# Kernel optimization log

Measured on AMD Instinct MI355X. Metric: run time of the kernel, lower is better.

Reference implementation:

```python
import math
import jax, jax.numpy as jnp
import numpy as np

N_EXPERTS = 8
TOP_K = 2
CAP_FACTOR = 1.25

def _capacity(num_tokens: int) -> int:
    cap = math.floor(TOP_K * CAP_FACTOR * num_tokens / N_EXPERTS)
    cap += cap % 2
    return max(int(cap), 2)

def setup_inputs() -> dict:
    key = jax.random.key(0)
    k1, k2 = jax.random.split(key)
    x = jax.random.normal(k1, (2, 2048, 1024), dtype=jnp.float32)
    w_gate = jax.random.normal(k2, (N_EXPERTS, 1024), dtype=jnp.float32) * 0.02
    return {"x": x, "w_gate": w_gate}

def reference(x, w_gate):
    B, S, D = x.shape
    N = B * S
    E, K = N_EXPERTS, TOP_K
    cap = _capacity(N)

    xf = x.astype(jnp.float32)
    router_logits = jnp.einsum('bsd,ed->bse', xf, w_gate)  # [B,S,E]
    lf = router_logits.reshape(N, E)

    # top-k gating: softmax over only the top-k logits (others -inf)
    topv, topi = jax.lax.top_k(lf, K)                       # [N,K]
    masked = jnp.full((N, E), -jnp.inf, dtype=lf.dtype)
    masked = masked.at[jnp.arange(N)[:, None], topi].set(topv)
    router_probs = jax.nn.softmax(masked, axis=-1)          # [N,E]

    # per-(k,token) expert one-hot, ranked by global cumsum order (k-major)
    mask = jax.nn.one_hot(topi, E, dtype=jnp.int32)         # [N,K,E]
    mask = jnp.transpose(mask, (1, 0, 2))                   # [K,N,E]
    rank = jnp.cumsum(mask.reshape(K * N, E), axis=0) - 1   # position within each expert
    rank = rank.reshape(K, N, E)
    mask = mask * (rank < cap)                              # drop tokens over capacity
    rank_k = jnp.sum(mask * rank, axis=-1)                  # [K,N] slot index per assignment

    weights = mask.astype(router_probs.dtype) * router_probs[None]   # [K,N,E]
    rank_oh = jax.nn.one_hot(rank_k, cap, dtype=router_probs.dtype)  # [K,N,cap]
    # sum over k of outer(weights[k,n,:], rank_oh[k,n,:]) -> [N,E,cap]
    expert_weights = jnp.einsum('kne,knc->nec', weights, rank_oh)
    expert_mask = expert_weights > 0                        # [N,E,cap] bool

    x_flat = x.reshape(N, D)
    # gather token features into expert batches: [E,cap,N] @ [N,D]
    expert_batches = jnp.einsum('nec,nd->ecd', expert_mask.astype(x.dtype), x_flat)

    return expert_weights, expert_mask, expert_batches, router_logits
```

## Files before the change

kernel.cpp:

```cpp
#include <hip/hip_runtime.h>
#include <hip/hip_bf16.h>
#include <math.h>

#define DIM 1024
#define NEXP 8

__global__ __launch_bounds__(256) void k_router(
    const float* __restrict__ x, const float* __restrict__ wg,
    float* __restrict__ logits,
    int* __restrict__ e1, int* __restrict__ e2,
    float* __restrict__ p1, float* __restrict__ p2, int N)
{
    __shared__ float wlds[NEXP * DIM];
    const int tid = threadIdx.x;
    for (int i = tid; i < NEXP * DIM; i += 256) wlds[i] = wg[i];
    __syncthreads();

    const int wave = tid >> 6, lane = tid & 63;
    const int n = blockIdx.x * 4 + wave;
    if (n >= N) return;

    const float4* x4 = (const float4*)x + (size_t)n * (DIM / 4);
    float s[NEXP];
#pragma unroll
    for (int e = 0; e < NEXP; ++e) s[e] = 0.0f;

#pragma unroll
    for (int i = 0; i < 4; ++i) {
        const int idx = lane + 64 * i;
        const float4 v = x4[idx];
#pragma unroll
        for (int e = 0; e < NEXP; ++e) {
            const float* wrow = &wlds[e * DIM + idx * 4];
            float acc = s[e];
            acc = fmaf(v.x, wrow[0], acc);
            acc = fmaf(v.y, wrow[1], acc);
            acc = fmaf(v.z, wrow[2], acc);
            acc = fmaf(v.w, wrow[3], acc);
            s[e] = acc;
        }
    }

#pragma unroll
    for (int off = 32; off >= 1; off >>= 1) {
#pragma unroll
        for (int e = 0; e < NEXP; ++e) s[e] += __shfl_xor(s[e], off, 64);
    }

    int be1 = 0; float bv1 = s[0];
#pragma unroll
    for (int e = 1; e < NEXP; ++e) { if (s[e] > bv1) { bv1 = s[e]; be1 = e; } }
    int be2 = -1; float bv2 = -INFINITY;
#pragma unroll
    for (int e = 0; e < NEXP; ++e) { if (e != be1 && s[e] > bv2) { bv2 = s[e]; be2 = e; } }

    const float t = expf(bv2 - bv1);
    const float inv = 1.0f / (1.0f + t);

    if (lane == 0) {
#pragma unroll
        for (int e = 0; e < NEXP; ++e) logits[(size_t)n * NEXP + e] = s[e];
        e1[n] = be1; e2[n] = be2;
        p1[n] = inv; p2[n] = t * inv;
    }
}

__global__ __launch_bounds__(1024) void k_scan(
    const int* __restrict__ e1, const int* __restrict__ e2,
    const float* __restrict__ p1, const float* __restrict__ p2,
    int* __restrict__ r_table, float* __restrict__ p_table,
    int* __restrict__ slot_token, int N, int cap)
{
    const int tid = threadIdx.x;
    for (int i = tid; i < N * NEXP; i += 1024) r_table[i] = -1;
    for (int i = tid; i < NEXP * cap; i += 1024) slot_token[i] = -1;
    __syncthreads();
    if (tid >= 64) return;

    const int lane = tid;
    const unsigned long long below =
        (lane == 0) ? 0ULL : ((~0ULL) >> (64 - lane));

    int cnt[NEXP];
#pragma unroll
    for (int q = 0; q < NEXP; ++q) cnt[q] = 0;

    const int rounds = N / 64;
    for (int k = 0; k < 2; ++k) {
        const int*   ee = (k == 0) ? e1 : e2;
        const float* pp = (k == 0) ? p1 : p2;
        for (int r = 0; r < rounds; ++r) {
            const int n = r * 64 + lane;
            const int e = ee[n];
            const float p = pp[n];
            int rank = 0x7fffffff;
#pragma unroll
            for (int q = 0; q < NEXP; ++q) {
                const unsigned long long bal = __ballot(e == q);
                if (e == q) rank = cnt[q] + __popcll(bal & below);
                cnt[q] += __popcll(bal);
            }
            if (rank < cap) {
                r_table[n * NEXP + e] = rank;
                p_table[n * NEXP + e] = p;
                slot_token[e * cap + rank] = n;
            }
        }
    }
}

__global__ __launch_bounds__(256) void k_fill_wm(
    const int* __restrict__ r_table, const float* __restrict__ p_table,
    float* __restrict__ W, float* __restrict__ M, int cap, int nrows)
{
    const int wave = threadIdx.x >> 6, lane = threadIdx.x & 63;
    const int row = blockIdx.x * 4 + wave;
    if (row >= nrows) return;

    const int r = r_table[row];
    const float p = p_table[row];
    const bool on = (r >= 0) && (p > 0.0f);

    if ((cap & 3) == 0) {
        float4* Wr = (float4*)(W + (size_t)row * cap);
        float4* Mr = (float4*)(M + (size_t)row * cap);
        const int nf4 = cap >> 2;
        for (int c4 = lane; c4 < nf4; c4 += 64) {
            const int c = c4 * 4;
            float4 w = make_float4(0.f, 0.f, 0.f, 0.f);
            float4 m = make_float4(0.f, 0.f, 0.f, 0.f);
            if (on) {
                const int d = r - c;
                if (d == 0)      { w.x = p; m.x = 1.f; }
                else if (d == 1) { w.y = p; m.y = 1.f; }
                else if (d == 2) { w.z = p; m.z = 1.f; }
                else if (d == 3) { w.w = p; m.w = 1.f; }
            }
            Wr[c4] = w; Mr[c4] = m;
        }
    } else {
        float* Wr = W + (size_t)row * cap;
        float* Mr = M + (size_t)row * cap;
        for (int c = lane; c < cap; c += 64) {
            const bool hit = on && (c == r);
            Wr[c] = hit ? p : 0.f;
            Mr[c] = hit ? 1.f : 0.f;
        }
    }
}

__global__ __launch_bounds__(256) void k_fill_batches(
    const int* __restrict__ slot_token, const float* __restrict__ x,
    float* __restrict__ Bt, int nrows)
{
    const int wave = threadIdx.x >> 6, lane = threadIdx.x & 63;
    const int row = blockIdx.x * 4 + wave;
    if (row >= nrows) return;

    const int tok = slot_token[row];
    float4* out = (float4*)(Bt + (size_t)row * DIM);
    if (tok >= 0) {
        const float4* src = (const float4*)(x + (size_t)tok * DIM);
#pragma unroll
        for (int i = 0; i < 4; ++i) out[lane + 64 * i] = src[lane + 64 * i];
    } else {
        const float4 z = make_float4(0.f, 0.f, 0.f, 0.f);
#pragma unroll
        for (int i = 0; i < 4; ++i) out[lane + 64 * i] = z;
    }
}

extern "C" void kernel_launch(void* const* d_in, const int* in_sizes, int n_in,
                              void* d_out, int out_size, void* d_ws, size_t ws_size,
                              hipStream_t stream)
{
    const float* x  = (const float*)d_in[0];
    const float* wg = (const float*)d_in[1];

    const int N = in_sizes[0] / DIM;
    int cap = (5 * N) / 16;
    cap += cap & 1;
    if (cap < 2) cap = 2;

    const size_t szW = (size_t)N * NEXP * cap;
    float* W  = (float*)d_out;
    float* M  = W + szW;
    float* Bt = M + szW;
    float* L  = Bt + (size_t)NEXP * cap * DIM;

    char* w = (char*)d_ws;
    int*   e1 = (int*)w;        w += (size_t)N * sizeof(int);
    int*   e2 = (int*)w;        w += (size_t)N * sizeof(int);
    float* p1 = (float*)w;      w += (size_t)N * sizeof(float);
    float* p2 = (float*)w;      w += (size_t)N * sizeof(float);
    int*   r_table = (int*)w;   w += (size_t)N * NEXP * sizeof(int);
    float* p_table = (float*)w; w += (size_t)N * NEXP * sizeof(float);
    int*   slot_token = (int*)w;

    k_router<<<(N + 3) / 4, 256, 0, stream>>>(x, wg, L, e1, e2, p1, p2, N);
    k_scan<<<1, 1024, 0, stream>>>(e1, e2, p1, p2, r_table, p_table,
                                   slot_token, N, cap);
    const int nrows_wm = N * NEXP;
    k_fill_wm<<<(nrows_wm + 3) / 4, 256, 0, stream>>>(r_table, p_table, W, M,
                                                      cap, nrows_wm);
    const int nrows_b = NEXP * cap;
    k_fill_batches<<<(nrows_b + 3) / 4, 256, 0, stream>>>(slot_token, x, Bt,
                                                          nrows_b);
}
```

Before: 474.0 us.

## Parallelize capacity scan across waves and fuse fill kernels

```diff
diff --git a/kernel.cpp b/kernel.cpp
--- a/kernel.cpp
+++ b/kernel.cpp
@@ -17,156 +17,170 @@
     __syncthreads();
 
     const int wave = tid >> 6, lane = tid & 63;
-    const int n = blockIdx.x * 4 + wave;
-    if (n >= N) return;
-
-    const float4* x4 = (const float4*)x + (size_t)n * (DIM / 4);
-    float s[NEXP];
-#pragma unroll
-    for (int e = 0; e < NEXP; ++e) s[e] = 0.0f;
-
-#pragma unroll
-    for (int i = 0; i < 4; ++i) {
-        const int idx = lane + 64 * i;
-        const float4 v = x4[idx];
-#pragma unroll
-        for (int e = 0; e < NEXP; ++e) {
-            const float* wrow = &wlds[e * DIM + idx * 4];
-            float acc = s[e];
-            acc = fmaf(v.x, wrow[0], acc);
-            acc = fmaf(v.y, wrow[1], acc);
-            acc = fmaf(v.z, wrow[2], acc);
-            acc = fmaf(v.w, wrow[3], acc);
-            s[e] = acc;
-        }
-    }
-
-#pragma unroll
-    for (int off = 32; off >= 1; off >>= 1) {
-#pragma unroll
-        for (int e = 0; e < NEXP; ++e) s[e] += __shfl_xor(s[e], off, 64);
-    }
-
-    int be1 = 0; float bv1 = s[0];
-#pragma unroll
-    for (int e = 1; e < NEXP; ++e) { if (s[e] > bv1) { bv1 = s[e]; be1 = e; } }
-    int be2 = -1; float bv2 = -INFINITY;
-#pragma unroll
-    for (int e = 0; e < NEXP; ++e) { if (e != be1 && s[e] > bv2) { bv2 = s[e]; be2 = e; } }
-
-    const float t = expf(bv2 - bv1);
-    const float inv = 1.0f / (1.0f + t);
-
-    if (lane == 0) {
-#pragma unroll
-        for (int e = 0; e < NEXP; ++e) logits[(size_t)n * NEXP + e] = s[e];
-        e1[n] = be1; e2[n] = be2;
-        p1[n] = inv; p2[n] = t * inv;
+
+    for (int t = 0; t < 4; ++t) {
+        const int n = blockIdx.x * 16 + wave * 4 + t;
+        if (n >= N) return;
+
+        const float4* x4 = (const float4*)x + (size_t)n * (DIM / 4);
+        float s[NEXP];
+#pragma unroll
+        for (int e = 0; e < NEXP; ++e) s[e] = 0.0f;
+
+#pragma unroll
+        for (int i = 0; i < 4; ++i) {
+            const int idx = lane + 64 * i;
+            const float4 v = x4[idx];
+#pragma unroll
+            for (int e = 0; e < NEXP; ++e) {
+                const float* wrow = &wlds[e * DIM + idx * 4];
+                float acc = s[e];
+                acc = fmaf(v.x, wrow[0], acc);
+                acc = fmaf(v.y, wrow[1], acc);
+                acc = fmaf(v.z, wrow[2], acc);
+                acc = fmaf(v.w, wrow[3], acc);
+                s[e] = acc;
+            }
+        }
+
+#pragma unroll
+        for (int off = 32; off >= 1; off >>= 1) {
+#pragma unroll
+            for (int e = 0; e < NEXP; ++e) s[e] += __shfl_xor(s[e], off, 64);
+        }
+
+        int be1 = 0; float bv1 = s[0];
+#pragma unroll
+        for (int e = 1; e < NEXP; ++e) { if (s[e] > bv1) { bv1 = s[e]; be1 = e; } }
+        int be2 = -1; float bv2 = -INFINITY;
+#pragma unroll
+        for (int e = 0; e < NEXP; ++e) { if (e != be1 && s[e] > bv2) { bv2 = s[e]; be2 = e; } }
+
+        const float tt = expf(bv2 - bv1);
+        const float inv = 1.0f / (1.0f + tt);
+
+        if (lane == 0) {
+#pragma unroll
+            for (int e = 0; e < NEXP; ++e) logits[(size_t)n * NEXP + e] = s[e];
+            e1[n] = be1; e2[n] = be2;
+            p1[n] = inv; p2[n] = tt * inv;
+        }
     }
 }
 
 __global__ __launch_bounds__(1024) void k_scan(
     const int* __restrict__ e1, const int* __restrict__ e2,
     const float* __restrict__ p1, const float* __restrict__ p2,
-    int* __restrict__ r_table, float* __restrict__ p_table,
+    int* __restrict__ r1, int* __restrict__ r2,
     int* __restrict__ slot_token, int N, int cap)
 {
+    __shared__ unsigned long long emask[128 * NEXP];
+    __shared__ int pre[128 * NEXP];
+
     const int tid = threadIdx.x;
-    for (int i = tid; i < N * NEXP; i += 1024) r_table[i] = -1;
+    const int wave = tid >> 6, lane = tid & 63;
+    const int cpk = N / 64;
+    const int nchunks = 2 * cpk;
+    const int nelem = nchunks * NEXP;
+
     for (int i = tid; i < NEXP * cap; i += 1024) slot_token[i] = -1;
+
+    for (int c = wave; c < nchunks; c += 16) {
+        const int k = c / cpk, r = c % cpk;
+        const int n = r * 64 + lane;
+        const int e = (k == 0 ? e1 : e2)[n];
+#pragma unroll
+        for (int q = 0; q < NEXP; ++q) {
+            const unsigned long long b = __ballot(e == q);
+            if (lane == q) emask[c * NEXP + q] = b;
+        }
+    }
     __syncthreads();
-    if (tid >= 64) return;
-
-    const int lane = tid;
+
+    if (tid < nelem) pre[tid] = (int)__popcll(emask[tid]);
+    __syncthreads();
+    for (int off = NEXP; off < nelem; off <<= 1) {
+        int add = 0;
+        if (tid < nelem && tid >= off) add = pre[tid - off];
+        __syncthreads();
+        if (tid < nelem) pre[tid] += add;
+        __syncthreads();
+    }
+
     const unsigned long long below =
         (lane == 0) ? 0ULL : ((~0ULL) >> (64 - lane));
-
-    int cnt[NEXP];
-#pragma unroll
-    for (int q = 0; q < NEXP; ++q) cnt[q] = 0;
-
-    const int rounds = N / 64;
-    for (int k = 0; k < 2; ++k) {
-        const int*   ee = (k == 0) ? e1 : e2;
-        const float* pp = (k == 0) ? p1 : p2;
-        for (int r = 0; r < rounds; ++r) {
-            const int n = r * 64 + lane;
-            const int e = ee[n];
-            const float p = pp[n];
-            int rank = 0x7fffffff;
-#pragma unroll
-            for (int q = 0; q < NEXP; ++q) {
-                const unsigned long long bal = __ballot(e == q);
-                if (e == q) rank = cnt[q] + __popcll(bal & below);
-                cnt[q] += __popcll(bal);
-            }
-            if (rank < cap) {
-                r_table[n * NEXP + e] = rank;
-                p_table[n * NEXP + e] = p;
-                slot_token[e * cap + rank] = n;
-            }
-        }
-    }
-}
-
-__global__ __launch_bounds__(256) void k_fill_wm(
-    const int* __restrict__ r_table, const float* __restrict__ p_table,
-    float* __restrict__ W, float* __restrict__ M, int cap, int nrows)
+    for (int c = wave; c < nchunks; c += 16) {
+        const int k = c / cpk, r = c % cpk;
+        const int n = r * 64 + lane;
+        const float p = (k == 0 ? p1 : p2)[n];
+        int e = 0; unsigned long long mm = 0;
+#pragma unroll
+        for (int q = 0; q < NEXP; ++q) {
+            const unsigned long long b = emask[c * NEXP + q];
+            if ((b >> lane) & 1ULL) { e = q; mm = b; }
+        }
+        const int bexc = (c > 0) ? pre[(c - 1) * NEXP + e] : 0;
+        const int rank = bexc + (int)__popcll(mm & below);
+        int* rout = (k == 0 ? r1 : r2);
+        if (rank < cap) {
+            rout[n] = rank;
+            slot_token[(size_t)e * cap + rank] = (p > 0.0f) ? n : -1;
+        } else {
+            rout[n] = -1;
+        }
+    }
+}
+
+__global__ __launch_bounds__(256) void k_fill(
+    const int* __restrict__ e1, const int* __restrict__ e2,
+    const float* __restrict__ p1, const float* __restrict__ p2,
+    const int* __restrict__ r1, const int* __restrict__ r2,
+    const int* __restrict__ slot_token, const float* __restrict__ x,
+    float* __restrict__ W, float* __restrict__ M, float* __restrict__ Bt,
+    int cap, int N, int nrows)
 {
     const int wave = threadIdx.x >> 6, lane = threadIdx.x & 63;
     const int row = blockIdx.x * 4 + wave;
     if (row >= nrows) return;
 
-    const int r = r_table[row];
-    const float p = p_table[row];
-    const bool on = (r >= 0) && (p > 0.0f);
-
-    if ((cap & 3) == 0) {
+    const int nwm = N * NEXP;
+    if (row < nwm) {
+        const int n = row >> 3, e = row & 7;
+        float p = 0.0f; int r = -1;
+        if (e == e1[n])      { r = r1[n]; p = p1[n]; }
+        else if (e == e2[n]) { r = r2[n]; p = p2[n]; }
+        const bool on = (r >= 0);
+
         float4* Wr = (float4*)(W + (size_t)row * cap);
         float4* Mr = (float4*)(M + (size_t)row * cap);
         const int nf4 = cap >> 2;
+        const float mval = (p > 0.0f) ? 1.0f : 0.0f;
         for (int c4 = lane; c4 < nf4; c4 += 64) {
             const int c = c4 * 4;
             float4 w = make_float4(0.f, 0.f, 0.f, 0.f);
             float4 m = make_float4(0.f, 0.f, 0.f, 0.f);
             if (on) {
                 const int d = r - c;
-                if (d == 0)      { w.x = p; m.x = 1.f; }
-                else if (d == 1) { w.y = p; m.y = 1.f; }
-                else if (d == 2) { w.z = p; m.z = 1.f; }
-                else if (d == 3) { w.w = p; m.w = 1.f; }
+                if (d == 0)      { w.x = p; m.x = mval; }
+                else if (d == 1) { w.y = p; m.y = mval; }
+                else if (d == 2) { w.z = p; m.z = mval; }
+                else if (d == 3) { w.w = p; m.w = mval; }
             }
             Wr[c4] = w; Mr[c4] = m;
         }
     } else {
-        float* Wr = W + (size_t)row * cap;
-        float* Mr = M + (size_t)row * cap;
-        for (int c = lane; c < cap; c += 64) {
-            const bool hit = on && (c == r);
-            Wr[c] = hit ? p : 0.f;
-            Mr[c] = hit ? 1.f : 0.f;
-        }
-    }
-}
-
-__global__ __launch_bounds__(256) void k_fill_batches(
-    const int* __restrict__ slot_token, const float* __restrict__ x,
-    float* __restrict__ Bt, int nrows)
-{
-    const int wave = threadIdx.x >> 6, lane = threadIdx.x & 63;
-    const int row = blockIdx.x * 4 + wave;
-    if (row >= nrows) return;
-
-    const int tok = slot_token[row];
-    float4* out = (float4*)(Bt + (size_t)row * DIM);
-    if (tok >= 0) {
-        const float4* src = (const float4*)(x + (size_t)tok * DIM);
-#pragma unroll
-        for (int i = 0; i < 4; ++i) out[lane + 64 * i] = src[lane + 64 * i];
-    } else {
-        const float4 z = make_float4(0.f, 0.f, 0.f, 0.f);
-#pragma unroll
-        for (int i = 0; i < 4; ++i) out[lane + 64 * i] = z;
+        const int brow = row - nwm;
+        const int tok = slot_token[brow];
+        float4* out = (float4*)(Bt + (size_t)brow * DIM);
+        if (tok >= 0) {
+            const float4* src = (const float4*)(x + (size_t)tok * DIM);
+#pragma unroll
+            for (int i = 0; i < 4; ++i) out[lane + 64 * i] = src[lane + 64 * i];
+        } else {
+            const float4 z = make_float4(0.f, 0.f, 0.f, 0.f);
+#pragma unroll
+            for (int i = 0; i < 4; ++i) out[lane + 64 * i] = z;
+        }
     }
 }
 
@@ -193,17 +207,14 @@
     int*   e2 = (int*)w;        w += (size_t)N * sizeof(int);
     float* p1 = (float*)w;      w += (size_t)N * sizeof(float);
     float* p2 = (float*)w;      w += (size_t)N * sizeof(float);
-    int*   r_table = (int*)w;   w += (size_t)N * NEXP * sizeof(int);
-    float* p_table = (float*)w; w += (size_t)N * NEXP * sizeof(float);
+    int*   r1 = (int*)w;        w += (size_t)N * sizeof(int);
+    int*   r2 = (int*)w;        w += (size_t)N * sizeof(int);
     int*   slot_token = (int*)w;
 
-    k_router<<<(N + 3) / 4, 256, 0, stream>>>(x, wg, L, e1, e2, p1, p2, N);
-    k_scan<<<1, 1024, 0, stream>>>(e1, e2, p1, p2, r_table, p_table,
-                                   slot_token, N, cap);
-    const int nrows_wm = N * NEXP;
-    k_fill_wm<<<(nrows_wm + 3) / 4, 256, 0, stream>>>(r_table, p_table, W, M,
-                                                      cap, nrows_wm);
-    const int nrows_b = NEXP * cap;
-    k_fill_batches<<<(nrows_b + 3) / 4, 256, 0, stream>>>(slot_token, x, Bt,
-                                                          nrows_b);
-}
+    k_router<<<(N + 15) / 16, 256, 0, stream>>>(x, wg, L, e1, e2, p1, p2, N);
+    k_scan<<<1, 1024, 0, stream>>>(e1, e2, p1, p2, r1, r2, slot_token, N, cap);
+    const int nrows = N * NEXP + NEXP * cap;
+    k_fill<<<(nrows + 3) / 4, 256, 0, stream>>>(e1, e2, p1, p2, r1, r2,
+                                                slot_token, x, W, M, Bt,
+                                                cap, N, nrows);
+}
```

New measurement: 406.6 us. 1.17x faster.
